# Kernel optimization log

Hardware: AMD Instinct MI355X
Metric: run time of the kernel (lower is better)

The kernel has to match this reference:

```python
import jax, jax.numpy as jnp
import numpy as np
import math
from jax import lax

# cfg['MODEL'] constants
MU = 0.1          # FISTA step size
LMBD = 0.1        # LAMBDA[0], sparsity weight
N_DICT = 1        # EXPANSION_FACTOR
N_STEPS = 6       # NUM_LAYERS (FISTA iterations)
K = 3             # kernel_size
PAD = 1           # padding
STRIDE = 1        # stride (POOLING=False, stride passed to conv)
DN = ('NCHW', 'OIHW', 'NCHW')


def _conv(x, w):
    # F.conv2d(x, w, stride=1, padding=PAD)
    return lax.conv_general_dilated(x, w, (STRIDE, STRIDE), [(PAD, PAD), (PAD, PAD)], dimension_numbers=DN)


def _conv_t(y, w):
    # F.conv_transpose2d(y, w, stride=1, padding=PAD) == conv2d with flipped, in/out-swapped kernel, pad K-1-PAD
    wt = jnp.transpose(jnp.flip(w, (-1, -2)), (1, 0, 2, 3))  # [Cin, Cout, K, K]
    p = K - 1 - PAD
    return lax.conv_general_dilated(y, wt, (1, 1), [(p, p), (p, p)], dimension_numbers=DN)


def _shrink(z, thr):
    # non_negative=True soft-threshold: relu(z - thr)
    return jax.nn.relu(z - thr)


def setup_inputs() -> dict:
    key = jax.random.key(0)
    k1, k2 = jax.random.split(key)
    x = jax.random.normal(k1, (16, 64, 56, 56), dtype=jnp.float32)
    # dictionary weight [out_channels, in_channels*n_dict, K, K], kaiming-ish scale
    W = jax.random.normal(k2, (128, 64 * N_DICT, K, K), dtype=jnp.float32) * 0.05
    return {"x": x, "W": W}


def reference(x, W):
    # w_norm: each output filter normalized to unit Frobenius norm
    Wn = W / jnp.sqrt(jnp.sum(W * W, axis=(1, 2, 3), keepdims=True) + 1e-12)
    thr = MU * LMBD
    xr = jnp.tile(x, (1, N_DICT, 1, 1)) if N_DICT > 1 else x

    # FISTA iteration 0: c = shrink(mu * D^T x)
    c = _shrink(MU * _conv(xr, Wn), thr)
    y = c
    c_prev = c
    t = 1.0
    for _ in range(N_STEPS - 1):
        r = xr - _conv_t(y, Wn)                       # residual x - D c
        c_new = _shrink(y + MU * _conv(r, Wn), thr)   # gradient step + shrink
        t_next = (1.0 + math.sqrt(1.0 + 4.0 * t * t)) / 2.0
        y = c_new + ((t - 1.0) / t_next) * (c_new - c_prev)  # momentum
        c_prev = c_new
        t = t_next
    # POOLING=False -> DictConv2d returns the sparse code directly
    return c_prev
```

## Files before the change

### kernel.cpp

```cpp
#include <hip/hip_runtime.h>
#include <hip/hip_bf16.h>
#include <math.h>

typedef __attribute__((ext_vector_type(8))) short short8;
typedef __attribute__((ext_vector_type(4))) float f32x4;

#define MU_  0.1f
#define THR_ 0.01f

static __device__ inline short f2bf(float f) {
    __hip_bfloat16 h = __float2bfloat16(f);
    return *reinterpret_cast<short*>(&h);
}
static __device__ inline float bf2f(unsigned short u) {
    unsigned int x = ((unsigned int)u) << 16;
    return __builtin_bit_cast(float, x);
}

#define ZB_ 5916

__global__ __launch_bounds__(256) void prep_kernel(
    const float* __restrict__ x, const float* __restrict__ W,
    float4* __restrict__ zbase, int n4,
    short* __restrict__ Xp, short* __restrict__ Wf2, short* __restrict__ Wt2) {
    __shared__ float lx[64 * 57];
    const int bid = blockIdx.x, tid = threadIdx.x;
    if (bid < ZB_) {
        int i = bid * 256 + tid;
        if (i < n4) zbase[i] = make_float4(0.f, 0.f, 0.f, 0.f);
    } else if (bid < ZB_ + 32) {
        int co = (bid - ZB_) * 4 + (tid >> 6);
        int ci = tid & 63;
        const float* wp = W + (co * 64 + ci) * 9;
        float v[9]; float s = 0.f;
#pragma unroll
        for (int t = 0; t < 9; ++t) { v[t] = wp[t]; s += v[t] * v[t]; }
#pragma unroll
        for (int off = 32; off; off >>= 1) s += __shfl_xor(s, off, 64);
        float inv = 1.0f / sqrtf(s + 1e-12f);
#pragma unroll
        for (int t = 0; t < 9; ++t) {
            Wf2[((t * 8 + (ci >> 3)) * 128 + co) * 8 + (ci & 7)] = f2bf(v[t] * inv);
            Wt2[((t * 16 + (co >> 3)) * 64 + ci) * 8 + (co & 7)] = f2bf(v[8 - t] * inv);
        }
    } else {
        int pb = bid - ZB_ - 32;
        int row = pb % 58, n = pb / 58;
        short* dst = Xp + ((size_t)(n * 58 + row) * 68) * 64;
        if (row >= 1 && row <= 56) {
            int h = row - 1;
            for (int j = tid; j < 64 * 56; j += 256) {
                int ci = j / 56, w = j - ci * 56;
                lx[ci * 57 + w] = x[((size_t)(n * 64 + ci)) * 3136 + h * 56 + w];
            }
            __syncthreads();
            for (int j = tid; j < 68 * 64; j += 256) {
                int s = j >> 6, ci = j & 63;
                float val = (s >= 2 && s < 58) ? lx[ci * 57 + (s - 2)] : 0.f;
                dst[(s << 6) + (ci ^ ((s & 7) << 3))] = f2bf(val);
            }
        } else {
            for (int j = tid; j < 68 * 64; j += 256) dst[j] = 0;
        }
    }
}

__global__ __launch_bounds__(256, 4) void conv_fwd(
    const short* __restrict__ inp,
    const short* __restrict__ Wf2,
    short* __restrict__ Yp,
    short* __restrict__ Cp,
    float* __restrict__ outp, int mode, float beta) {
    __shared__ __align__(16) short smem[14688];
    const int bid = blockIdx.x, tid = threadIdx.x;
    const int cb = bid >= 896;
    const int q = bid - cb * 896;
    const int sid = (q & 7) * 112 + (q >> 3);
    const int n = sid / 56, r = sid - n * 56 + 1;
    {
        const short8* src = (const short8*)(inp + ((size_t)(n * 58 + (r - 1)) * 68) * 64);
        for (int j = tid; j < 1632; j += 256) {
            int srow = j >> 3, w = j & 7;
            *(short8*)(smem + srow * 72 + w * 8) = src[j];
        }
    }
    const int lane = tid & 63, ct = tid >> 6, quad = lane >> 4, l15 = lane & 15;
    const int co = cb * 64 + ct * 16 + l15;
    const size_t prow = ((size_t)(n * 58 + r) * 68) * 128;

    short8 yold8[2], cold8[2];
    int pvv[2], pg[2]; bool pok[2];
#pragma unroll
    for (int k = 0; k < 2; ++k) {
        int item = tid + k * 256;
        pok[k] = item < 448;
        pvv[k] = item >> 3; pg[k] = item & 7;
        if (mode != 0 && pok[k]) {
            int s = pvv[k] + 2;
            size_t off = prow + (size_t)s * 128 + 8 * ((pg[k] + 8 * cb) ^ (s & 7));
            yold8[k] = *(const short8*)(Yp + off);
            if (mode == 1) cold8[k] = *(const short8*)(Cp + off);
        }
    }
    __syncthreads();

    f32x4 acc[4];
#pragma unroll
    for (int pt = 0; pt < 4; ++pt) acc[pt] = (f32x4){0.f, 0.f, 0.f, 0.f};

#pragma unroll
    for (int hp = 0; hp < 2; ++hp) {
        short8 Areg[9];
#pragma unroll
        for (int i = 0; i < 9; ++i) {
            int f = hp * 9 + i, t = f >> 1, half = f & 1;
            Areg[i] = *(const short8*)(Wf2 +
                ((size_t)((t * 8 + half * 4 + quad) * 128 + co)) * 8);
        }
#pragma unroll
        for (int i = 0; i < 9; ++i) {
            const int f = hp * 9 + i, t = f >> 1, half = f & 1;
            const int dh = t / 3, dw = t % 3;
            const int u = l15 + dw + 1;
            const int phys = (half * 4 + quad) ^ (u & 7);
            const int base = (dh * 68 + u) * 72 + phys * 8;
#pragma unroll
            for (int pt = 0; pt < 4; ++pt) {
                short8 bv = *(const short8*)(smem + base + pt * 1152);
                acc[pt] = __builtin_amdgcn_mfma_f32_16x16x32_bf16(Areg[i], bv, acc[pt], 0, 0, 0);
            }
        }
    }

    __syncthreads();
    short* tb_y = smem;
    short* tb_c = smem + 4608;
    if (mode != 0) {
#pragma unroll
        for (int k = 0; k < 2; ++k) if (pok[k]) {
            int o = pvv[k] * 72 + 8 * (pg[k] ^ (pvv[k] & 3));
            *(short8*)(tb_y + o) = yold8[k];
            if (mode == 1) *(short8*)(tb_c + o) = cold8[k];
        }
    }
    __syncthreads();
    const int h = r - 1;
#pragma unroll
    for (int pt = 0; pt < 4; ++pt) {
        const int px = pt * 16 + l15;
#pragma unroll
        for (int reg = 0; reg < 4; ++reg) {
            const int lch = ct * 16 + quad * 4 + reg;
            const int slot = px * 72 + (lch ^ ((px & 3) << 3));
            const float a = acc[pt][reg];
            if (mode == 0) {
                float c = fmaxf(MU_ * a - THR_, 0.f);
                short cb16 = f2bf(c);
                tb_y[slot] = cb16;
                tb_c[slot] = cb16;
            } else if (mode == 1) {
                float yold = bf2f((unsigned short)tb_y[slot]);
                float cold = bf2f((unsigned short)tb_c[slot]);
                float c = fmaxf(yold + MU_ * a - THR_, 0.f);
                tb_y[slot] = f2bf(c + beta * (c - cold));
                tb_c[slot] = f2bf(c);
            } else {
                if (px < 56) {
                    float yold = bf2f((unsigned short)tb_y[slot]);
                    float c = fmaxf(yold + MU_ * a - THR_, 0.f);
                    outp[((size_t)(n * 128 + cb * 64 + lch)) * 3136 + h * 56 + px] = c;
                }
            }
        }
    }
    if (mode != 2) {
        __syncthreads();
        for (int item = tid; item < 448; item += 256) {
            int vv = item >> 3, g = item & 7;
            int so = vv * 72 + 8 * (g ^ (vv & 3));
            short8 yv = *(const short8*)(tb_y + so);
            short8 cv = *(const short8*)(tb_c + so);
            int s = vv + 2;
            size_t off = prow + (size_t)s * 128 + 8 * ((g + 8 * cb) ^ (s & 7));
            *(short8*)(Yp + off) = yv;
            *(short8*)(Cp + off) = cv;
        }
    }
}

__global__ __launch_bounds__(256, 4) void conv_t(
    const short* __restrict__ Ypb,
    const short* __restrict__ Wt2,
    const short* __restrict__ Xp,
    short* __restrict__ Rp) {
    __shared__ __align__(16) short smem[14688];
    const int bid = blockIdx.x, tid = threadIdx.x;
    const int sid = (bid & 7) * 112 + (bid >> 3);
    const int n = sid / 56, r = sid - n * 56 + 1;
    const int lane = tid & 63, ct = tid >> 6, quad = lane >> 4, l15 = lane & 15;
    const int ci = ct * 16 + l15;
    const short8* src = (const short8*)(Ypb + ((size_t)(n * 58 + (r - 1)) * 68) * 128);
    const size_t prow = ((size_t)(n * 58 + r) * 68) * 64;

    short8 xold8[2];
    int pvv[2], pg[2]; bool pok[2];
#pragma unroll
    for (int k = 0; k < 2; ++k) {
        int item = tid + k * 256;
        pok[k] = item < 448;
        pvv[k] = item >> 3; pg[k] = item & 7;
        if (pok[k]) {
            int s = pvv[k] + 2;
            xold8[k] = *(const short8*)(Xp + prow + (size_t)s * 64 + 8 * (pg[k] ^ (s & 7)));
        }
    }

    f32x4 acc[4];
#pragma unroll
    for (int pt = 0; pt < 4; ++pt) acc[pt] = (f32x4){0.f, 0.f, 0.f, 0.f};

#pragma unroll
    for (int p = 0; p < 2; ++p) {
        if (p) __syncthreads();
        for (int j = tid; j < 1632; j += 256) {
            int srow = j >> 3, w = j & 7;
            *(short8*)(smem + srow * 72 + w * 8) = src[srow * 16 + p * 8 + w];
        }
        __syncthreads();
#pragma unroll
        for (int sub = 0; sub < 2; ++sub) {
            short8 Areg[9];
#pragma unroll
            for (int i = 0; i < 9; ++i) {
                int f = sub * 9 + i, t = f >> 1, sh = f & 1;
                Areg[i] = *(const short8*)(Wt2 +
                    ((size_t)((t * 16 + (p * 2 + sh) * 4 + quad) * 64 + ci)) * 8);
            }
#pragma unroll
            for (int i = 0; i < 9; ++i) {
                const int f = sub * 9 + i, t = f >> 1, sh = f & 1;
                const int dh = t / 3, dw = t % 3;
                const int u = l15 + dw + 1;
                const int phys = (sh * 4 + quad) ^ (u & 7);
                const int base = (dh * 68 + u) * 72 + phys * 8;
#pragma unroll
                for (int pt = 0; pt < 4; ++pt) {
                    short8 bv = *(const short8*)(smem + base + pt * 1152);
                    acc[pt] = __builtin_amdgcn_mfma_f32_16x16x32_bf16(Areg[i], bv, acc[pt], 0, 0, 0);
                }
            }
        }
    }

    __syncthreads();
    short* tb = smem;
#pragma unroll
    for (int k = 0; k < 2; ++k) if (pok[k]) {
        *(short8*)(tb + pvv[k] * 72 + 8 * (pg[k] ^ (pvv[k] & 3))) = xold8[k];
    }
    __syncthreads();
#pragma unroll
    for (int pt = 0; pt < 4; ++pt) {
        const int px = pt * 16 + l15;
#pragma unroll
        for (int reg = 0; reg < 4; ++reg) {
            const int cir = ct * 16 + quad * 4 + reg;
            const int slot = px * 72 + (cir ^ ((px & 3) << 3));
            float xo = bf2f((unsigned short)tb[slot]);
            tb[slot] = f2bf(xo - acc[pt][reg]);
        }
    }
    __syncthreads();
    for (int item = tid; item < 448; item += 256) {
        int vv = item >> 3, g = item & 7;
        short8 val = *(const short8*)(tb + vv * 72 + 8 * (g ^ (vv & 3)));
        int s = vv + 2;
        *(short8*)(Rp + prow + (size_t)s * 64 + 8 * (g ^ (s & 7))) = val;
    }
}

extern "C" void kernel_launch(void* const* d_in, const int* in_sizes, int n_in,
                              void* d_out, int out_size, void* d_ws, size_t ws_size,
                              hipStream_t stream) {
    const float* x = (const float*)d_in[0];
    const float* W = (const float*)d_in[1];
    float* out = (float*)d_out;

    const size_t XPN = (size_t)16 * 58 * 68 * 64;
    const size_t YPN = 2 * XPN;
    short* Xp = (short*)d_ws;
    short* Rp = Xp + XPN;
    short* Yp = Rp + XPN;
    short* Cp = Yp + YPN;
    short* Wf2 = Cp + YPN;
    short* Wt2 = Wf2 + 73728;

    const int n4 = (int)((XPN + YPN) * 2 / 16);
    const int prep_blocks = ZB_ + 32 + 58 * 16;
    hipLaunchKernelGGL(prep_kernel, dim3(prep_blocks), dim3(256), 0, stream,
                       x, W, (float4*)Rp, n4, Xp, Wf2, Wt2);

    dim3 b(256, 1, 1);
    hipLaunchKernelGGL(conv_fwd, dim3(1792), b, 0, stream, Xp, Wf2, Yp, Cp,
                       (float*)nullptr, 0, 0.f);
    double t = 1.0;
    for (int it = 1; it <= 5; ++it) {
        hipLaunchKernelGGL(conv_t, dim3(896), b, 0, stream, Yp, Wt2, Xp, Rp);
        double tn = (1.0 + sqrt(1.0 + 4.0 * t * t)) / 2.0;
        float beta = (float)((t - 1.0) / tn);
        hipLaunchKernelGGL(conv_fwd, dim3(1792), b, 0, stream, Rp, Wf2, Yp, Cp,
                           (it == 5) ? out : (float*)nullptr, (it == 5) ? 2 : 1,
                           beta);
        t = tn;
    }
}
```

Measured before the change: 359.1 us.

## Compute all output channels per block and reorder MFMA loops for B-fragment reuse

conv_fwd now has each block handle all 128 output channels for one image row instead of splitting channels across two blocks, which halves the grid and avoids staging the input row into shared memory twice. Each wave takes a 2-pixel-tile by 4-channel-tile sub-block, so one LDS B fragment feeds four MFMAs and fewer LDS reads are needed per MFMA. conv_t gets the same reorder, with each wave owning one pixel tile across four input-channel tiles. In exchange each block runs twice as long, the epilogue runs in two channel halves with extra barriers, and the weight fragments are reloaded per tap instead of being held in registers.

```diff
diff --git a/kernel.cpp b/kernel.cpp
--- a/kernel.cpp
+++ b/kernel.cpp
@@ -73,9 +73,7 @@
     float* __restrict__ outp, int mode, float beta) {
     __shared__ __align__(16) short smem[14688];
     const int bid = blockIdx.x, tid = threadIdx.x;
-    const int cb = bid >= 896;
-    const int q = bid - cb * 896;
-    const int sid = (q & 7) * 112 + (q >> 3);
+    const int sid = (bid & 7) * 112 + (bid >> 3);
     const int n = sid / 56, r = sid - n * 56 + 1;
     {
         const short8* src = (const short8*)(inp + ((size_t)(n * 58 + (r - 1)) * 68) * 64);
@@ -85,7 +83,7 @@
         }
     }
     const int lane = tid & 63, ct = tid >> 6, quad = lane >> 4, l15 = lane & 15;
-    const int co = cb * 64 + ct * 16 + l15;
+    const int cog = ct & 1, pxg = ct >> 1;
     const size_t prow = ((size_t)(n * 58 + r) * 68) * 128;
 
     short8 yold8[2], cold8[2];
@@ -97,94 +95,114 @@
         pvv[k] = item >> 3; pg[k] = item & 7;
         if (mode != 0 && pok[k]) {
             int s = pvv[k] + 2;
-            size_t off = prow + (size_t)s * 128 + 8 * ((pg[k] + 8 * cb) ^ (s & 7));
+            size_t off = prow + (size_t)s * 128 + 8 * (pg[k] ^ (s & 7));
             yold8[k] = *(const short8*)(Yp + off);
             if (mode == 1) cold8[k] = *(const short8*)(Cp + off);
         }
     }
     __syncthreads();
 
-    f32x4 acc[4];
-#pragma unroll
-    for (int pt = 0; pt < 4; ++pt) acc[pt] = (f32x4){0.f, 0.f, 0.f, 0.f};
-
-#pragma unroll
-    for (int hp = 0; hp < 2; ++hp) {
-        short8 Areg[9];
-#pragma unroll
-        for (int i = 0; i < 9; ++i) {
-            int f = hp * 9 + i, t = f >> 1, half = f & 1;
-            Areg[i] = *(const short8*)(Wf2 +
+    f32x4 acc[2][4];
+#pragma unroll
+    for (int pt = 0; pt < 2; ++pt)
+#pragma unroll
+        for (int cot = 0; cot < 4; ++cot) acc[pt][cot] = (f32x4){0.f, 0.f, 0.f, 0.f};
+
+#pragma unroll
+    for (int f = 0; f < 18; ++f) {
+        const int t = f >> 1, half = f & 1;
+        const int dh = t / 3, dw = t % 3;
+        const int u = l15 + dw + 1;
+        const int phys = (half * 4 + quad) ^ (u & 7);
+        short8 areg[4];
+#pragma unroll
+        for (int cot = 0; cot < 4; ++cot) {
+            const int co = cog * 64 + cot * 16 + l15;
+            areg[cot] = *(const short8*)(Wf2 +
                 ((size_t)((t * 8 + half * 4 + quad) * 128 + co)) * 8);
         }
 #pragma unroll
-        for (int i = 0; i < 9; ++i) {
-            const int f = hp * 9 + i, t = f >> 1, half = f & 1;
-            const int dh = t / 3, dw = t % 3;
-            const int u = l15 + dw + 1;
-            const int phys = (half * 4 + quad) ^ (u & 7);
-            const int base = (dh * 68 + u) * 72 + phys * 8;
-#pragma unroll
-            for (int pt = 0; pt < 4; ++pt) {
-                short8 bv = *(const short8*)(smem + base + pt * 1152);
-                acc[pt] = __builtin_amdgcn_mfma_f32_16x16x32_bf16(Areg[i], bv, acc[pt], 0, 0, 0);
-            }
+        for (int pt = 0; pt < 2; ++pt) {
+            const int pti = pxg * 2 + pt;
+            const short8 bv = *(const short8*)(smem +
+                (dh * 68 + pti * 16 + u) * 72 + phys * 8);
+#pragma unroll
+            for (int cot = 0; cot < 4; ++cot)
+                acc[pt][cot] = __builtin_amdgcn_mfma_f32_16x16x32_bf16(areg[cot], bv, acc[pt][cot], 0, 0, 0);
         }
     }
 
     __syncthreads();
     short* tb_y = smem;
     short* tb_c = smem + 4608;
-    if (mode != 0) {
-#pragma unroll
-        for (int k = 0; k < 2; ++k) if (pok[k]) {
-            int o = pvv[k] * 72 + 8 * (pg[k] ^ (pvv[k] & 3));
-            *(short8*)(tb_y + o) = yold8[k];
-            if (mode == 1) *(short8*)(tb_c + o) = cold8[k];
-        }
-    }
-    __syncthreads();
     const int h = r - 1;
 #pragma unroll
-    for (int pt = 0; pt < 4; ++pt) {
-        const int px = pt * 16 + l15;
-#pragma unroll
-        for (int reg = 0; reg < 4; ++reg) {
-            const int lch = ct * 16 + quad * 4 + reg;
-            const int slot = px * 72 + (lch ^ ((px & 3) << 3));
-            const float a = acc[pt][reg];
-            if (mode == 0) {
-                float c = fmaxf(MU_ * a - THR_, 0.f);
-                short cb16 = f2bf(c);
-                tb_y[slot] = cb16;
-                tb_c[slot] = cb16;
-            } else if (mode == 1) {
-                float yold = bf2f((unsigned short)tb_y[slot]);
-                float cold = bf2f((unsigned short)tb_c[slot]);
-                float c = fmaxf(yold + MU_ * a - THR_, 0.f);
-                tb_y[slot] = f2bf(c + beta * (c - cold));
-                tb_c[slot] = f2bf(c);
-            } else {
-                if (px < 56) {
-                    float yold = bf2f((unsigned short)tb_y[slot]);
-                    float c = fmaxf(yold + MU_ * a - THR_, 0.f);
-                    outp[((size_t)(n * 128 + cb * 64 + lch)) * 3136 + h * 56 + px] = c;
+    for (int hh = 0; hh < 2; ++hh) {
+        if (mode != 0) {
+#pragma unroll
+            for (int k = 0; k < 2; ++k) if (pok[k]) {
+                int o = pvv[k] * 72 + 8 * (pg[k] ^ (pvv[k] & 3));
+                *(short8*)(tb_y + o) = yold8[k];
+                if (mode == 1) *(short8*)(tb_c + o) = cold8[k];
+            }
+        }
+        __syncthreads();
+        if (hh == 0 && mode != 0) {
+#pragma unroll
+            for (int k = 0; k < 2; ++k) if (pok[k]) {
+                int s = pvv[k] + 2;
+                size_t off = prow + (size_t)s * 128 + 8 * ((pg[k] + 8) ^ (s & 7));
+                yold8[k] = *(const short8*)(Yp + off);
+                if (mode == 1) cold8[k] = *(const short8*)(Cp + off);
+            }
+        }
+        if (cog == hh) {
+#pragma unroll
+            for (int pt = 0; pt < 2; ++pt) {
+                const int px = pxg * 32 + pt * 16 + l15;
+#pragma unroll
+                for (int cot = 0; cot < 4; ++cot) {
+#pragma unroll
+                    for (int reg = 0; reg < 4; ++reg) {
+                        const int lch = cot * 16 + quad * 4 + reg;
+                        const int slot = px * 72 + (lch ^ ((px & 3) << 3));
+                        const float a = acc[pt][cot][reg];
+                        if (mode == 0) {
+                            float c = fmaxf(MU_ * a - THR_, 0.f);
+                            short cb16 = f2bf(c);
+                            tb_y[slot] = cb16;
+                            tb_c[slot] = cb16;
+                        } else if (mode == 1) {
+                            float yold = bf2f((unsigned short)tb_y[slot]);
+                            float cold = bf2f((unsigned short)tb_c[slot]);
+                            float c = fmaxf(yold + MU_ * a - THR_, 0.f);
+                            tb_y[slot] = f2bf(c + beta * (c - cold));
+                            tb_c[slot] = f2bf(c);
+                        } else {
+                            if (px < 56) {
+                                float yold = bf2f((unsigned short)tb_y[slot]);
+                                float c = fmaxf(yold + MU_ * a - THR_, 0.f);
+                                outp[((size_t)(n * 128 + hh * 64 + lch)) * 3136 + h * 56 + px] = c;
+                            }
+                        }
+                    }
                 }
             }
         }
-    }
-    if (mode != 2) {
-        __syncthreads();
-        for (int item = tid; item < 448; item += 256) {
-            int vv = item >> 3, g = item & 7;
-            int so = vv * 72 + 8 * (g ^ (vv & 3));
-            short8 yv = *(const short8*)(tb_y + so);
-            short8 cv = *(const short8*)(tb_c + so);
-            int s = vv + 2;
-            size_t off = prow + (size_t)s * 128 + 8 * ((g + 8 * cb) ^ (s & 7));
-            *(short8*)(Yp + off) = yv;
-            *(short8*)(Cp + off) = cv;
-        }
+        if (mode != 2) {
+            __syncthreads();
+            for (int item = tid; item < 448; item += 256) {
+                int vv = item >> 3, g = item & 7;
+                int so = vv * 72 + 8 * (g ^ (vv & 3));
+                short8 yv = *(const short8*)(tb_y + so);
+                short8 cv = *(const short8*)(tb_c + so);
+                int s = vv + 2;
+                size_t off = prow + (size_t)s * 128 + 8 * ((g + 8 * hh) ^ (s & 7));
+                *(short8*)(Yp + off) = yv;
+                *(short8*)(Cp + off) = cv;
+            }
+        }
+        if (hh == 0) __syncthreads();
     }
 }
 
@@ -198,7 +216,6 @@
     const int sid = (bid & 7) * 112 + (bid >> 3);
     const int n = sid / 56, r = sid - n * 56 + 1;
     const int lane = tid & 63, ct = tid >> 6, quad = lane >> 4, l15 = lane & 15;
-    const int ci = ct * 16 + l15;
     const short8* src = (const short8*)(Ypb + ((size_t)(n * 58 + (r - 1)) * 68) * 128);
     const size_t prow = ((size_t)(n * 58 + r) * 68) * 64;
 
@@ -217,7 +234,7 @@
 
     f32x4 acc[4];
 #pragma unroll
-    for (int pt = 0; pt < 4; ++pt) acc[pt] = (f32x4){0.f, 0.f, 0.f, 0.f};
+    for (int cit = 0; cit < 4; ++cit) acc[cit] = (f32x4){0.f, 0.f, 0.f, 0.f};
 
 #pragma unroll
     for (int p = 0; p < 2; ++p) {
@@ -228,27 +245,23 @@
         }
         __syncthreads();
 #pragma unroll
-        for (int sub = 0; sub < 2; ++sub) {
-            short8 Areg[9];
-#pragma unroll
-            for (int i = 0; i < 9; ++i) {
-                int f = sub * 9 + i, t = f >> 1, sh = f & 1;
-                Areg[i] = *(const short8*)(Wt2 +
+        for (int f = 0; f < 18; ++f) {
+            const int t = f >> 1, sh = f & 1;
+            const int dh = t / 3, dw = t % 3;
+            const int u = l15 + dw + 1;
+            const int phys = (sh * 4 + quad) ^ (u & 7);
+            short8 areg[4];
+#pragma unroll
+            for (int cit = 0; cit < 4; ++cit) {
+                const int ci = cit * 16 + l15;
+                areg[cit] = *(const short8*)(Wt2 +
                     ((size_t)((t * 16 + (p * 2 + sh) * 4 + quad) * 64 + ci)) * 8);
             }
-#pragma unroll
-            for (int i = 0; i < 9; ++i) {
-                const int f = sub * 9 + i, t = f >> 1, sh = f & 1;
-                const int dh = t / 3, dw = t % 3;
-                const int u = l15 + dw + 1;
-                const int phys = (sh * 4 + quad) ^ (u & 7);
-                const int base = (dh * 68 + u) * 72 + phys * 8;
-#pragma unroll
-                for (int pt = 0; pt < 4; ++pt) {
-                    short8 bv = *(const short8*)(smem + base + pt * 1152);
-                    acc[pt] = __builtin_amdgcn_mfma_f32_16x16x32_bf16(Areg[i], bv, acc[pt], 0, 0, 0);
-                }
-            }
+            const short8 bv = *(const short8*)(smem +
+                (dh * 68 + ct * 16 + u) * 72 + phys * 8);
+#pragma unroll
+            for (int cit = 0; cit < 4; ++cit)
+                acc[cit] = __builtin_amdgcn_mfma_f32_16x16x32_bf16(areg[cit], bv, acc[cit], 0, 0, 0);
         }
     }
 
@@ -259,15 +272,17 @@
         *(short8*)(tb + pvv[k] * 72 + 8 * (pg[k] ^ (pvv[k] & 3))) = xold8[k];
     }
     __syncthreads();
-#pragma unroll
-    for (int pt = 0; pt < 4; ++pt) {
-        const int px = pt * 16 + l15;
-#pragma unroll
-        for (int reg = 0; reg < 4; ++reg) {
-            const int cir = ct * 16 + quad * 4 + reg;
-            const int slot = px * 72 + (cir ^ ((px & 3) << 3));
-            float xo = bf2f((unsigned short)tb[slot]);
-            tb[slot] = f2bf(xo - acc[pt][reg]);
+    {
+        const int px = ct * 16 + l15;
+#pragma unroll
+        for (int cit = 0; cit < 4; ++cit) {
+#pragma unroll
+            for (int reg = 0; reg < 4; ++reg) {
+                const int cir = cit * 16 + quad * 4 + reg;
+                const int slot = px * 72 + (cir ^ ((px & 3) << 3));
+                float xo = bf2f((unsigned short)tb[slot]);
+                tb[slot] = f2bf(xo - acc[cit][reg]);
+            }
         }
     }
     __syncthreads();
@@ -301,14 +316,14 @@
                        x, W, (float4*)Rp, n4, Xp, Wf2, Wt2);
 
     dim3 b(256, 1, 1);
-    hipLaunchKernelGGL(conv_fwd, dim3(1792), b, 0, stream, Xp, Wf2, Yp, Cp,
+    hipLaunchKernelGGL(conv_fwd, dim3(896), b, 0, stream, Xp, Wf2, Yp, Cp,
                        (float*)nullptr, 0, 0.f);
     double t = 1.0;
     for (int it = 1; it <= 5; ++it) {
         hipLaunchKernelGGL(conv_t, dim3(896), b, 0, stream, Yp, Wt2, Xp, Rp);
         double tn = (1.0 + sqrt(1.0 + 4.0 * t * t)) / 2.0;
         float beta = (float)((t - 1.0) / tn);
-        hipLaunchKernelGGL(conv_fwd, dim3(1792), b, 0, stream, Rp, Wf2, Yp, Cp,
+        hipLaunchKernelGGL(conv_fwd, dim3(896), b, 0, stream, Rp, Wf2, Yp, Cp,
                            (it == 5) ? out : (float*)nullptr, (it == 5) ? 2 : 1,
                            beta);
         t = tn;
```

Measured after the change: 358.4 us. About the same (-0.2%).
